# Optimization experiments

Hardware: AMD Instinct MI355X
Metric: run time of the kernel (lower is better)

## Reference

```python
import jax, jax.numpy as jnp
import numpy as np

H = 8          # num_heads
D = 64         # out_dims = input_dims / num_heads
DM = H * D     # input_dims = 512
B, S = 2, 2048


def _linear(x, W, b):
    # torch nn.Linear: x @ W.T + b, W: [out, in]
    return jnp.einsum('...d,ed->...e', x, W) + b


def setup_inputs() -> dict:
    key = jax.random.key(0)
    ks = jax.random.split(key, 12)
    inp = {
        'query': jax.random.normal(ks[0], (B, S, DM), dtype=jnp.float32),
        'key': jax.random.normal(ks[1], (B, S, DM), dtype=jnp.float32),
        'value': jax.random.normal(ks[2], (B, S, DM), dtype=jnp.float32),
        'Wq': jax.random.normal(ks[3], (D, D), dtype=jnp.float32) * 0.02,
        'bq': jnp.zeros((D,), dtype=jnp.float32),
        'Wk': jax.random.normal(ks[4], (D, D), dtype=jnp.float32) * 0.02,
        'bk': jnp.zeros((D,), dtype=jnp.float32),
        'Wv': jax.random.normal(ks[5], (D, D), dtype=jnp.float32) * 0.02,
        'bv': jnp.zeros((D,), dtype=jnp.float32),
        'Wo': jax.random.normal(ks[6], (DM, DM), dtype=jnp.float32) * 0.02,
        'bo': jnp.zeros((DM,), dtype=jnp.float32),
        'mask': jax.random.randint(ks[7], (B, 1, 1, S), 0, 2, dtype=jnp.int32),
    }
    return inp


def reference(query, key, value, Wq, bq, Wk, bk, Wv, bv, Wo, bo, mask):
    b, qlen = query.shape[0], query.shape[1]
    klen = key.shape[1]
    # split heads: [B, S, H, D]
    q = _linear(query.reshape(b, qlen, H, D), Wq, bq)
    k = _linear(key.reshape(b, klen, H, D), Wk, bk)
    v = _linear(value.reshape(b, klen, H, D), Wv, bv)
    # scores: [B, H, Q, K]
    attn = jnp.einsum('bqhd,bkhd->bhqk', q, k)
    attn = jnp.where(mask == 0, jnp.float32(-1e20), attn)
    # NOTE: original scale is num_heads ** 1 / 2 == H / 2 (Python precedence quirk)
    score = jax.nn.softmax(attn * (2.0 / H), axis=-1)
    # out einsum gives [B, Q, D, H]; flattening gives (d, h) feature order
    out = jnp.einsum('bhqv,bvhd->bqdh', score, v)
    out = out.reshape(b, qlen, D * H)
    return _linear(out, Wo, bo)
```

## Files before the change

### kernel.cpp

```cpp
#include <hip/hip_runtime.h>
#include <math.h>

typedef float f32x4 __attribute__((ext_vector_type(4)));
typedef short s16x8 __attribute__((ext_vector_type(8)));
typedef unsigned short ushort_t;

namespace {
constexpr int kH  = 8;
constexpr int kD  = 64;
constexpr int kDM = 512;
constexpr int kB  = 2;
constexpr int kS  = 2048;
constexpr size_t kNE = (size_t)kB * kS * kDM;
constexpr size_t kNL = (size_t)kB * kH * kS;
}

__device__ __forceinline__ void split_bf16(float x, ushort_t& hi, ushort_t& lo) {
  union { float f; unsigned u; } a; a.f = x;
  hi = (ushort_t)(a.u >> 16);
  union { unsigned u; float f; } hh; hh.u = a.u & 0xffff0000u;
  union { float f; unsigned u; } r; r.f = x - hh.f;
  lo = (ushort_t)(r.u >> 16);
}
__device__ __forceinline__ ushort_t rne_bf16(float x) {
  union { float f; unsigned u; } a; a.f = x;
  const unsigned t = a.u + 0x7fffu + ((a.u >> 16) & 1u);
  return (ushort_t)(t >> 16);
}
__device__ __forceinline__ float bf_to_f(unsigned u16) {
  union { unsigned u; float f; } a; a.u = u16 << 16; return a.f;
}

__global__ __launch_bounds__(256)
void w_split_kernel(const float* __restrict__ Wo, const float* __restrict__ Wq,
                    const float* __restrict__ Wk, const float* __restrict__ Wv,
                    ushort_t* __restrict__ wo_h, ushort_t* __restrict__ wo_l,
                    ushort_t* __restrict__ wq_h, ushort_t* __restrict__ wq_l,
                    ushort_t* __restrict__ wk_h, ushort_t* __restrict__ wk_l,
                    ushort_t* __restrict__ wv_h, ushort_t* __restrict__ wv_l) {
  const int bid = blockIdx.x;
  if (bid < 128) {
    const int gi = (bid * 256 + threadIdx.x) * 8;
    const int e  = gi >> 9;
    const int g0 = gi & 511;
    const int fbase = (g0 & 63) * 8 + (g0 >> 6);
    ushort_t h[8], l[8];
    #pragma unroll
    for (int j = 0; j < 8; ++j)
      split_bf16(Wo[(size_t)e * kDM + fbase + j * 8], h[j], l[j]);
    int4 hp, lp;
    hp.x = (int)((unsigned)h[0] | ((unsigned)h[1] << 16));
    hp.y = (int)((unsigned)h[2] | ((unsigned)h[3] << 16));
    hp.z = (int)((unsigned)h[4] | ((unsigned)h[5] << 16));
    hp.w = (int)((unsigned)h[6] | ((unsigned)h[7] << 16));
    lp.x = (int)((unsigned)l[0] | ((unsigned)l[1] << 16));
    lp.y = (int)((unsigned)l[2] | ((unsigned)l[3] << 16));
    lp.z = (int)((unsigned)l[4] | ((unsigned)l[5] << 16));
    lp.w = (int)((unsigned)l[6] | ((unsigned)l[7] << 16));
    *(int4*)&wo_h[(size_t)e * kDM + g0] = hp;
    *(int4*)&wo_l[(size_t)e * kDM + g0] = lp;
  } else {
    const int which = bid - 128;
    const float* W = (which == 0) ? Wq : (which == 1) ? Wk : Wv;
    ushort_t* oh = (which == 0) ? wq_h : (which == 1) ? wk_h : wv_h;
    ushort_t* ol = (which == 0) ? wq_l : (which == 1) ? wk_l : wv_l;
    #pragma unroll
    for (int cc = 0; cc < 4; ++cc) {
      const int i = (cc * 256 + threadIdx.x) * 4;
      const float4 v = *(const float4*)&W[i];
      ushort_t h[4], l[4];
      split_bf16(v.x, h[0], l[0]);
      split_bf16(v.y, h[1], l[1]);
      split_bf16(v.z, h[2], l[2]);
      split_bf16(v.w, h[3], l[3]);
      int2 hp, lp;
      hp.x = (int)((unsigned)h[0] | ((unsigned)h[1] << 16));
      hp.y = (int)((unsigned)h[2] | ((unsigned)h[3] << 16));
      lp.x = (int)((unsigned)l[0] | ((unsigned)l[1] << 16));
      lp.y = (int)((unsigned)l[2] | ((unsigned)l[3] << 16));
      *(int2*)&oh[i] = hp;
      *(int2*)&ol[i] = lp;
    }
  }
}

__global__ __launch_bounds__(256, 2)
void kv_proj_kernel(const float* __restrict__ xk, const float* __restrict__ xv,
                    const ushort_t* __restrict__ wk_h, const ushort_t* __restrict__ wk_l,
                    const float* __restrict__ bk,
                    const ushort_t* __restrict__ wv_h, const ushort_t* __restrict__ wv_l,
                    const float* __restrict__ bv,
                    ushort_t* __restrict__ k_hi, ushort_t* __restrict__ vt_hi) {
  __shared__ __align__(16) ushort_t Xh[64][72];
  __shared__ __align__(16) ushort_t Xl[64][72];
  const int which = blockIdx.z;
  const float* x = which ? xv : xk;
  const ushort_t* wh = which ? wv_h : wk_h;
  const ushort_t* wl = which ? wv_l : wk_l;
  const float* bias = which ? bv : bk;
  const int h = blockIdx.y;
  const int t0g = blockIdx.x * 64;
  const int b = t0g >> 11, s0 = t0g & (kS - 1);
  const int tid  = threadIdx.x;
  const int w    = tid >> 6;
  const int lane = tid & 63;
  const int ln   = lane & 15;
  const int quad = lane >> 4;
  const size_t hb = ((size_t)b * kH + h) * (size_t)(kS * kD);

  #pragma unroll
  for (int cc = 0; cc < 4; ++cc) {
    const int id = tid + cc * 256;
    const int r = id >> 4, c = id & 15;
    const float4 v = *(const float4*)&x[((size_t)t0g + r) * kDM + h * kD + c * 4];
    ushort_t hh[4], ll[4];
    split_bf16(v.x, hh[0], ll[0]);
    split_bf16(v.y, hh[1], ll[1]);
    split_bf16(v.z, hh[2], ll[2]);
    split_bf16(v.w, hh[3], ll[3]);
    int2 hp, lp;
    hp.x = (int)((unsigned)hh[0] | ((unsigned)hh[1] << 16));
    hp.y = (int)((unsigned)hh[2] | ((unsigned)hh[3] << 16));
    lp.x = (int)((unsigned)ll[0] | ((unsigned)ll[1] << 16));
    lp.y = (int)((unsigned)ll[2] | ((unsigned)ll[3] << 16));
    *(int2*)&Xh[r][c * 4] = hp;
    *(int2*)&Xl[r][c * 4] = lp;
  }
  __syncthreads();

  f32x4 C[4];
  #pragma unroll
  for (int eb = 0; eb < 4; ++eb) C[eb] = (f32x4){0.f, 0.f, 0.f, 0.f};
  #pragma unroll
  for (int kc = 0; kc < 2; ++kc) {
    const s16x8 ah = *(const s16x8*)&Xh[w * 16 + ln][kc * 32 + quad * 8];
    const s16x8 al = *(const s16x8*)&Xl[w * 16 + ln][kc * 32 + quad * 8];
    s16x8 bh[4], bl[4];
    #pragma unroll
    for (int eb = 0; eb < 4; ++eb) {
      bh[eb] = *(const s16x8*)&wh[(size_t)(eb * 16 + ln) * kD + kc * 32 + quad * 8];
      bl[eb] = *(const s16x8*)&wl[(size_t)(eb * 16 + ln) * kD + kc * 32 + quad * 8];
    }
    #pragma unroll
    for (int eb = 0; eb < 4; ++eb)
      C[eb] = __builtin_amdgcn_mfma_f32_16x16x32_bf16(ah, bh[eb], C[eb], 0, 0, 0);
    #pragma unroll
    for (int eb = 0; eb < 4; ++eb)
      C[eb] = __builtin_amdgcn_mfma_f32_16x16x32_bf16(ah, bl[eb], C[eb], 0, 0, 0);
    #pragma unroll
    for (int eb = 0; eb < 4; ++eb)
      C[eb] = __builtin_amdgcn_mfma_f32_16x16x32_bf16(al, bh[eb], C[eb], 0, 0, 0);
  }
  __syncthreads();

  if (which == 0) {
    #pragma unroll
    for (int eb = 0; eb < 4; ++eb) {
      const float be = bias[eb * 16 + ln];
      #pragma unroll
      for (int r = 0; r < 4; ++r)
        Xh[w * 16 + quad * 4 + r][eb * 16 + ln] = rne_bf16(C[eb][r] + be);
    }
    __syncthreads();
    #pragma unroll
    for (int cc = 0; cc < 2; ++cc) {
      const int id = tid + cc * 256;
      const int r = id >> 3, c = id & 7;
      *(int4*)&k_hi[hb + (size_t)(s0 + r) * kD + c * 8] = *(int4*)&Xh[r][c * 8];
    }
  } else {
    #pragma unroll
    for (int eb = 0; eb < 4; ++eb) {
      const float be = bias[eb * 16 + ln];
      #pragma unroll
      for (int r = 0; r < 4; ++r)
        Xh[eb * 16 + ln][w * 16 + quad * 4 + r] = rne_bf16(C[eb][r] + be);
    }
    __syncthreads();
    #pragma unroll
    for (int cc = 0; cc < 2; ++cc) {
      const int id = tid + cc * 256;
      const int r = id >> 3, c = id & 7;
      *(int4*)&vt_hi[hb + (size_t)r * kS + s0 + c * 8] = *(int4*)&Xh[r][c * 8];
    }
  }
}

__global__ __launch_bounds__(256, 4)
void attn_kernel(const float* __restrict__ xq,
                 const ushort_t* __restrict__ wq_h, const ushort_t* __restrict__ wq_l,
                 const float* __restrict__ bq,
                 const ushort_t* __restrict__ k_hi, const ushort_t* __restrict__ vt_hi,
                 const int* __restrict__ mask,
                 ushort_t* __restrict__ Opart, float* __restrict__ lws) {
  __shared__ __align__(16) ushort_t smem[128 * 72];
  __shared__ __align__(16) ushort_t Pbm[4 * 32 * 40];
  __shared__ float Mz[64];
  ushort_t (*QT)[72] = (ushort_t(*)[72])smem;
  ushort_t (*Kh)[72] = (ushort_t(*)[72])smem;
  ushort_t (*Vh)[72] = (ushort_t(*)[72])(smem + 64 * 72);
  ushort_t (*Pb)[32][40] = (ushort_t(*)[32][40])Pbm;

  const int tid  = threadIdx.x;
  const int w    = tid >> 6;
  const int lane = tid & 63;
  const int ln   = lane & 15;
  const int quad = lane >> 4;
  const int h    = blockIdx.y;
  const int b    = blockIdx.z >> 2;
  const int quarter = blockIdx.z & 3;
  const int q0   = blockIdx.x * 128;
  const size_t hb = ((size_t)b * kH + h) * (size_t)(kS * kD);

  s16x8 aqh[2][2];
  #pragma unroll
  for (int g = 0; g < 2; ++g) {
    const int qrow = q0 + w * 32 + g * 16 + ln;
    f32x4 C[4];
    #pragma unroll
    for (int eb = 0; eb < 4; ++eb) C[eb] = (f32x4){0.f, 0.f, 0.f, 0.f};
    #pragma unroll
    for (int kc = 0; kc < 2; ++kc) {
      const float* xp = &xq[((size_t)b * kS + qrow) * kDM + h * kD + kc * 32 + quad * 8];
      const float4 x0 = *(const float4*)xp;
      const float4 x1 = *(const float4*)(xp + 4);
      const float xs[8] = {x0.x, x0.y, x0.z, x0.w, x1.x, x1.y, x1.z, x1.w};
      s16x8 ah, al;
      #pragma unroll
      for (int j = 0; j < 8; ++j) {
        ushort_t hi, lo;
        split_bf16(xs[j], hi, lo);
        ah[j] = (short)hi; al[j] = (short)lo;
      }
      #pragma unroll
      for (int eb = 0; eb < 4; ++eb) {
        const s16x8 bh = *(const s16x8*)&wq_h[(size_t)(eb * 16 + ln) * kD + kc * 32 + quad * 8];
        const s16x8 bl = *(const s16x8*)&wq_l[(size_t)(eb * 16 + ln) * kD + kc * 32 + quad * 8];
        C[eb] = __builtin_amdgcn_mfma_f32_16x16x32_bf16(ah, bh, C[eb], 0, 0, 0);
        C[eb] = __builtin_amdgcn_mfma_f32_16x16x32_bf16(ah, bl, C[eb], 0, 0, 0);
        C[eb] = __builtin_amdgcn_mfma_f32_16x16x32_bf16(al, bh, C[eb], 0, 0, 0);
      }
    }
    #pragma unroll
    for (int eb = 0; eb < 4; ++eb) {
      const float be = bq[eb * 16 + ln];
      #pragma unroll
      for (int r = 0; r < 4; ++r)
        QT[w * 32 + g * 16 + quad * 4 + r][eb * 16 + ln] = rne_bf16(C[eb][r] + be);
    }
    #pragma unroll
    for (int db = 0; db < 2; ++db)
      aqh[g][db] = *(const s16x8*)&QT[w * 32 + g * 16 + ln][db * 32 + quad * 8];
  }
  __syncthreads();

  f32x4 O[2][4];
  #pragma unroll
  for (int g = 0; g < 2; ++g)
    #pragma unroll
    for (int db = 0; db < 4; ++db) O[g][db] = (f32x4){0.f, 0.f, 0.f, 0.f};
  float rs[2][4] = {};

  const int kt0 = quarter * 8;
  for (int kt = kt0; kt < kt0 + 8; ++kt) {
    __syncthreads();
    {
      const ushort_t* gkh = k_hi + hb + (size_t)kt * 64 * kD;
      const ushort_t* gvh = vt_hi + hb + (size_t)kt * 64;
      #pragma unroll
      for (int cc = 0; cc < 2; ++cc) {
        const int id = tid + cc * 256;
        const int r = id >> 3, c = id & 7;
        *(int4*)&Kh[r][c * 8] = *(const int4*)&gkh[r * kD + c * 8];
        *(int4*)&Vh[r][c * 8] = *(const int4*)&gvh[(size_t)r * kS + c * 8];
      }
      if (tid < 64) Mz[tid] = (mask[(size_t)b * kS + kt * 64 + tid] != 0) ? 1.0f : 0.0f;
    }
    __syncthreads();

    #pragma unroll
    for (int h32 = 0; h32 < 2; ++h32) {
      f32x4 C[2][2];
      #pragma unroll
      for (int g = 0; g < 2; ++g) {
        C[g][0] = (f32x4){0.f, 0.f, 0.f, 0.f};
        C[g][1] = (f32x4){0.f, 0.f, 0.f, 0.f};
      }
      #pragma unroll
      for (int db = 0; db < 2; ++db) {
        const s16x8 bh0 = *(const s16x8*)&Kh[h32 * 32 + ln][db * 32 + quad * 8];
        const s16x8 bh1 = *(const s16x8*)&Kh[h32 * 32 + 16 + ln][db * 32 + quad * 8];
        #pragma unroll
        for (int g = 0; g < 2; ++g) {
          C[g][0] = __builtin_amdgcn_mfma_f32_16x16x32_bf16(aqh[g][db], bh0, C[g][0], 0, 0, 0);
          C[g][1] = __builtin_amdgcn_mfma_f32_16x16x32_bf16(aqh[g][db], bh1, C[g][1], 0, 0, 0);
        }
      }
      #pragma unroll
      for (int g = 0; g < 2; ++g) {
        #pragma unroll
        for (int kb = 0; kb < 2; ++kb) {
          const float mz = Mz[h32 * 32 + kb * 16 + ln];
          #pragma unroll
          for (int r = 0; r < 4; ++r) {
            const float p = mz * __expf(0.25f * C[g][kb][r]);
            union { float f; unsigned u; } pa; pa.f = p;
            const unsigned t = pa.u + 0x7fffu + ((pa.u >> 16) & 1u);
            Pb[w][g * 16 + quad * 4 + r][kb * 16 + ln] = (ushort_t)(t >> 16);
            union { unsigned u; float f; } pr; pr.u = t & 0xffff0000u;
            rs[g][r] += pr.f;
          }
        }
      }
      {
        const s16x8 ph0 = *(const s16x8*)&Pb[w][ln][quad * 8];
        const s16x8 ph1 = *(const s16x8*)&Pb[w][16 + ln][quad * 8];
        #pragma unroll
        for (int db = 0; db < 4; ++db) {
          const s16x8 vh = *(const s16x8*)&Vh[db * 16 + ln][h32 * 32 + quad * 8];
          O[0][db] = __builtin_amdgcn_mfma_f32_16x16x32_bf16(ph0, vh, O[0][db], 0, 0, 0);
          O[1][db] = __builtin_amdgcn_mfma_f32_16x16x32_bf16(ph1, vh, O[1][db], 0, 0, 0);
        }
      }
    }
  }

  #pragma unroll
  for (int m = 1; m < 16; m <<= 1) {
    #pragma unroll
    for (int g = 0; g < 2; ++g)
      #pragma unroll
      for (int r = 0; r < 4; ++r) rs[g][r] += __shfl_xor(rs[g][r], m);
  }
  if (ln == 0) {
    #pragma unroll
    for (int g = 0; g < 2; ++g) {
      float* lp = lws + (size_t)quarter * kNL + ((size_t)b * kH + h) * kS +
                  q0 + w * 32 + g * 16 + quad * 4;
      #pragma unroll
      for (int r = 0; r < 4; ++r) lp[r] = rs[g][r];
    }
  }

  __syncthreads();
  #pragma unroll
  for (int g = 0; g < 2; ++g)
    #pragma unroll
    for (int db = 0; db < 4; ++db)
      #pragma unroll
      for (int r = 0; r < 4; ++r)
        QT[w * 32 + g * 16 + quad * 4 + r][db * 16 + ln] = rne_bf16(O[g][db][r]);
  __syncthreads();
  ushort_t* op = Opart + (size_t)quarter * kNE;
  #pragma unroll
  for (int cc = 0; cc < 4; ++cc) {
    const int id = tid + cc * 256;
    const int r = id >> 3, c = id & 7;
    *(int4*)&op[((size_t)b * kS + q0 + r) * kDM + h * kD + c * 8] = *(int4*)&QT[r][c * 8];
  }
}

__global__ __launch_bounds__(256, 2)
void out_proj_kernel(const ushort_t* __restrict__ Opart, const float* __restrict__ lws,
                     const ushort_t* __restrict__ wh, const ushort_t* __restrict__ wl,
                     const float* __restrict__ bo, float* __restrict__ out) {
  __shared__ __align__(16) ushort_t Ah[64][72];
  __shared__ __align__(16) ushort_t Al[64][72];
  __shared__ __align__(16) ushort_t Bh[64][72];
  __shared__ __align__(16) ushort_t Bl[64][72];
  __shared__ float linv[kH][64];
  const int t0 = blockIdx.x * 64;
  const int e0 = blockIdx.y * 64;
  const int b  = t0 >> 11;
  const int s0 = t0 & (kS - 1);
  const int tid  = threadIdx.x;
  const int w    = tid >> 6;
  const int lane = tid & 63;
  const int ln   = lane & 15;
  const int quad = lane >> 4;

  for (int id = tid; id < kH * 64; id += 256) {
    const int hh = id >> 6, r = id & 63;
    const size_t base = ((size_t)b * kH + hh) * kS + s0 + r;
    linv[hh][r] = 1.0f / (lws[base] + lws[kNL + base] +
                          lws[2 * kNL + base] + lws[3 * kNL + base]);
  }

  f32x4 C[4];
  #pragma unroll
  for (int eb = 0; eb < 4; ++eb) C[eb] = (f32x4){0.f, 0.f, 0.f, 0.f};

  for (int k0 = 0; k0 < kDM; k0 += 64) {
    __syncthreads();
    const int hh = k0 >> 6;
    #pragma unroll
    for (int cc = 0; cc < 4; ++cc) {
      const int id = tid + cc * 256;
      const int r = id >> 4, c4 = id & 15;
      const size_t off = (size_t)(t0 + r) * kDM + k0 + c4 * 4;
      float a0 = 0.f, a1 = 0.f, a2 = 0.f, a3 = 0.f;
      #pragma unroll
      for (int q = 0; q < 4; ++q) {
        const int2 u = *(const int2*)&Opart[(size_t)q * kNE + off];
        a0 += bf_to_f((unsigned)u.x & 0xffffu);
        a1 += bf_to_f((unsigned)u.x >> 16);
        a2 += bf_to_f((unsigned)u.y & 0xffffu);
        a3 += bf_to_f((unsigned)u.y >> 16);
      }
      const float li = linv[hh][r];
      a0 *= li; a1 *= li; a2 *= li; a3 *= li;
      ushort_t h4[4], l4[4];
      split_bf16(a0, h4[0], l4[0]);
      split_bf16(a1, h4[1], l4[1]);
      split_bf16(a2, h4[2], l4[2]);
      split_bf16(a3, h4[3], l4[3]);
      int2 hp, lp;
      hp.x = (int)((unsigned)h4[0] | ((unsigned)h4[1] << 16));
      hp.y = (int)((unsigned)h4[2] | ((unsigned)h4[3] << 16));
      lp.x = (int)((unsigned)l4[0] | ((unsigned)l4[1] << 16));
      lp.y = (int)((unsigned)l4[2] | ((unsigned)l4[3] << 16));
      *(int2*)&Ah[r][c4 * 4] = hp;
      *(int2*)&Al[r][c4 * 4] = lp;
    }
    #pragma unroll
    for (int cc = 0; cc < 2; ++cc) {
      const int id = tid + cc * 256;
      const int r = id >> 3, off = (id & 7) * 8;
      *(int4*)&Bh[r][off] = *(const int4*)&wh[(size_t)(e0 + r) * kDM + k0 + off];
      *(int4*)&Bl[r][off] = *(const int4*)&wl[(size_t)(e0 + r) * kDM + k0 + off];
    }
    __syncthreads();
    #pragma unroll
    for (int kc = 0; kc < 2; ++kc) {
      const s16x8 ah = *(const s16x8*)&Ah[w * 16 + ln][kc * 32 + quad * 8];
      const s16x8 al = *(const s16x8*)&Al[w * 16 + ln][kc * 32 + quad * 8];
      s16x8 bh[4], bl[4];
      #pragma unroll
      for (int eb = 0; eb < 4; ++eb) {
        bh[eb] = *(const s16x8*)&Bh[eb * 16 + ln][kc * 32 + quad * 8];
        bl[eb] = *(const s16x8*)&Bl[eb * 16 + ln][kc * 32 + quad * 8];
      }
      #pragma unroll
      for (int eb = 0; eb < 4; ++eb)
        C[eb] = __builtin_amdgcn_mfma_f32_16x16x32_bf16(ah, bh[eb], C[eb], 0, 0, 0);
      #pragma unroll
      for (int eb = 0; eb < 4; ++eb)
        C[eb] = __builtin_amdgcn_mfma_f32_16x16x32_bf16(ah, bl[eb], C[eb], 0, 0, 0);
      #pragma unroll
      for (int eb = 0; eb < 4; ++eb)
        C[eb] = __builtin_amdgcn_mfma_f32_16x16x32_bf16(al, bh[eb], C[eb], 0, 0, 0);
    }
  }

  #pragma unroll
  for (int eb = 0; eb < 4; ++eb) {
    const int e = e0 + eb * 16 + ln;
    const float be = bo[e];
    #pragma unroll
    for (int r = 0; r < 4; ++r) {
      const int t = t0 + w * 16 + quad * 4 + r;
      out[(size_t)t * kDM + e] = C[eb][r] + be;
    }
  }
}

extern "C" void kernel_launch(void* const* d_in, const int* in_sizes, int n_in,
                              void* d_out, int out_size, void* d_ws, size_t ws_size,
                              hipStream_t stream) {
  const float* query = (const float*)d_in[0];
  const float* key   = (const float*)d_in[1];
  const float* value = (const float*)d_in[2];
  const float* Wq = (const float*)d_in[3];
  const float* bq = (const float*)d_in[4];
  const float* Wk = (const float*)d_in[5];
  const float* bk = (const float*)d_in[6];
  const float* Wv = (const float*)d_in[7];
  const float* bv = (const float*)d_in[8];
  const float* Wo = (const float*)d_in[9];
  const float* bo = (const float*)d_in[10];
  const int* mask = (const int*)d_in[11];
  float* out = (float*)d_out;

  ushort_t* k_hi  = (ushort_t*)d_ws;
  ushort_t* vt_hi = k_hi + kNE;
  ushort_t* wo_h  = vt_hi + kNE;
  ushort_t* wo_l  = wo_h + (size_t)kDM * kDM;
  ushort_t* Opart = wo_l + (size_t)kDM * kDM;
  float*    lws   = (float*)(Opart + 4 * kNE);
  ushort_t* wq_h  = (ushort_t*)(lws + 4 * kNL);
  ushort_t* wq_l  = wq_h + kD * kD;
  ushort_t* wk_h  = wq_l + kD * kD;
  ushort_t* wk_l  = wk_h + kD * kD;
  ushort_t* wv_h  = wk_l + kD * kD;
  ushort_t* wv_l  = wv_h + kD * kD;

  w_split_kernel<<<dim3(131), 256, 0, stream>>>(
      Wo, Wq, Wk, Wv, wo_h, wo_l, wq_h, wq_l, wk_h, wk_l, wv_h, wv_l);
  kv_proj_kernel<<<dim3(kB * kS / 64, kH, 2), 256, 0, stream>>>(
      key, value, wk_h, wk_l, bk, wv_h, wv_l, bv, k_hi, vt_hi);
  attn_kernel<<<dim3(kS / 128, kH, kB * 4), 256, 0, stream>>>(
      query, wq_h, wq_l, bq, k_hi, vt_hi, mask, Opart, lws);
  out_proj_kernel<<<dim3(kB * kS / 64, kDM / 64), 256, 0, stream>>>(
      Opart, lws, wo_h, wo_l, bo, out);
}
```

Before: 173.6 us.

## Fold weight split into KV projection, drop LDS staging in attention, retile out-proj

Removes the separate weight-split launch by handling the Wo/Wq splitting in an extra z-slice of the KV projection kernel, which now splits Wk/Wv to bf16 hi/lo on the fly from fp32. The attention kernel stops staging K, V and the mask through shared memory with block barriers and reads MFMA fragments straight from global memory. The output projection is retiled to 32x128 tiles with a 32-wide k-step. Together these aim to cut launch overhead and synchronization, at the cost of uncoalesced, redundant global loads in attention and more k-loop iterations in the out-projection.

After: 242.2 us. 1.4x slower.

```diff
diff --git a/kernel.cpp b/kernel.cpp
--- a/kernel.cpp
+++ b/kernel.cpp
@@ -31,72 +31,63 @@
   union { unsigned u; float f; } a; a.u = u16 << 16; return a.f;
 }
 
-__global__ __launch_bounds__(256)
-void w_split_kernel(const float* __restrict__ Wo, const float* __restrict__ Wq,
-                    const float* __restrict__ Wk, const float* __restrict__ Wv,
+__global__ __launch_bounds__(256, 2)
+void kv_proj_kernel(const float* __restrict__ xk, const float* __restrict__ xv,
+                    const float* __restrict__ Wk, const float* __restrict__ bk,
+                    const float* __restrict__ Wv, const float* __restrict__ bv,
+                    const float* __restrict__ Wo, const float* __restrict__ Wq,
                     ushort_t* __restrict__ wo_h, ushort_t* __restrict__ wo_l,
                     ushort_t* __restrict__ wq_h, ushort_t* __restrict__ wq_l,
-                    ushort_t* __restrict__ wk_h, ushort_t* __restrict__ wk_l,
-                    ushort_t* __restrict__ wv_h, ushort_t* __restrict__ wv_l) {
-  const int bid = blockIdx.x;
-  if (bid < 128) {
-    const int gi = (bid * 256 + threadIdx.x) * 8;
-    const int e  = gi >> 9;
-    const int g0 = gi & 511;
-    const int fbase = (g0 & 63) * 8 + (g0 >> 6);
-    ushort_t h[8], l[8];
-    #pragma unroll
-    for (int j = 0; j < 8; ++j)
-      split_bf16(Wo[(size_t)e * kDM + fbase + j * 8], h[j], l[j]);
-    int4 hp, lp;
-    hp.x = (int)((unsigned)h[0] | ((unsigned)h[1] << 16));
-    hp.y = (int)((unsigned)h[2] | ((unsigned)h[3] << 16));
-    hp.z = (int)((unsigned)h[4] | ((unsigned)h[5] << 16));
-    hp.w = (int)((unsigned)h[6] | ((unsigned)h[7] << 16));
-    lp.x = (int)((unsigned)l[0] | ((unsigned)l[1] << 16));
-    lp.y = (int)((unsigned)l[2] | ((unsigned)l[3] << 16));
-    lp.z = (int)((unsigned)l[4] | ((unsigned)l[5] << 16));
-    lp.w = (int)((unsigned)l[6] | ((unsigned)l[7] << 16));
-    *(int4*)&wo_h[(size_t)e * kDM + g0] = hp;
-    *(int4*)&wo_l[(size_t)e * kDM + g0] = lp;
-  } else {
-    const int which = bid - 128;
-    const float* W = (which == 0) ? Wq : (which == 1) ? Wk : Wv;
-    ushort_t* oh = (which == 0) ? wq_h : (which == 1) ? wk_h : wv_h;
-    ushort_t* ol = (which == 0) ? wq_l : (which == 1) ? wk_l : wv_l;
-    #pragma unroll
-    for (int cc = 0; cc < 4; ++cc) {
-      const int i = (cc * 256 + threadIdx.x) * 4;
-      const float4 v = *(const float4*)&W[i];
-      ushort_t h[4], l[4];
-      split_bf16(v.x, h[0], l[0]);
-      split_bf16(v.y, h[1], l[1]);
-      split_bf16(v.z, h[2], l[2]);
-      split_bf16(v.w, h[3], l[3]);
-      int2 hp, lp;
-      hp.x = (int)((unsigned)h[0] | ((unsigned)h[1] << 16));
-      hp.y = (int)((unsigned)h[2] | ((unsigned)h[3] << 16));
-      lp.x = (int)((unsigned)l[0] | ((unsigned)l[1] << 16));
-      lp.y = (int)((unsigned)l[2] | ((unsigned)l[3] << 16));
-      *(int2*)&oh[i] = hp;
-      *(int2*)&ol[i] = lp;
-    }
-  }
-}
-
-__global__ __launch_bounds__(256, 2)
-void kv_proj_kernel(const float* __restrict__ xk, const float* __restrict__ xv,
-                    const ushort_t* __restrict__ wk_h, const ushort_t* __restrict__ wk_l,
-                    const float* __restrict__ bk,
-                    const ushort_t* __restrict__ wv_h, const ushort_t* __restrict__ wv_l,
-                    const float* __restrict__ bv,
                     ushort_t* __restrict__ k_hi, ushort_t* __restrict__ vt_hi) {
+  const int which = blockIdx.z;
+  if (which == 2) {
+    const int bid = blockIdx.y * 64 + blockIdx.x;
+    if (bid < 128) {
+      const int gi = (bid * 256 + threadIdx.x) * 8;
+      const int e  = gi >> 9;
+      const int g0 = gi & 511;
+      const int fbase = (g0 & 63) * 8 + (g0 >> 6);
+      ushort_t h8[8], l8[8];
+      #pragma unroll
+      for (int j = 0; j < 8; ++j)
+        split_bf16(Wo[(size_t)e * kDM + fbase + j * 8], h8[j], l8[j]);
+      int4 hp, lp;
+      hp.x = (int)((unsigned)h8[0] | ((unsigned)h8[1] << 16));
+      hp.y = (int)((unsigned)h8[2] | ((unsigned)h8[3] << 16));
+      hp.z = (int)((unsigned)h8[4] | ((unsigned)h8[5] << 16));
+      hp.w = (int)((unsigned)h8[6] | ((unsigned)h8[7] << 16));
+      lp.x = (int)((unsigned)l8[0] | ((unsigned)l8[1] << 16));
+      lp.y = (int)((unsigned)l8[2] | ((unsigned)l8[3] << 16));
+      lp.z = (int)((unsigned)l8[4] | ((unsigned)l8[5] << 16));
+      lp.w = (int)((unsigned)l8[6] | ((unsigned)l8[7] << 16));
+      *(int4*)&wo_h[(size_t)e * kDM + g0] = hp;
+      *(int4*)&wo_l[(size_t)e * kDM + g0] = lp;
+    } else if (bid == 128) {
+      #pragma unroll
+      for (int cc = 0; cc < 4; ++cc) {
+        const int i = (cc * 256 + threadIdx.x) * 4;
+        const float4 v = *(const float4*)&Wq[i];
+        ushort_t h4[4], l4[4];
+        split_bf16(v.x, h4[0], l4[0]);
+        split_bf16(v.y, h4[1], l4[1]);
+        split_bf16(v.z, h4[2], l4[2]);
+        split_bf16(v.w, h4[3], l4[3]);
+        int2 hp, lp;
+        hp.x = (int)((unsigned)h4[0] | ((unsigned)h4[1] << 16));
+        hp.y = (int)((unsigned)h4[2] | ((unsigned)h4[3] << 16));
+        lp.x = (int)((unsigned)l4[0] | ((unsigned)l4[1] << 16));
+        lp.y = (int)((unsigned)l4[2] | ((unsigned)l4[3] << 16));
+        *(int2*)&wq_h[i] = hp;
+        *(int2*)&wq_l[i] = lp;
+      }
+    }
+    return;
+  }
+
   __shared__ __align__(16) ushort_t Xh[64][72];
   __shared__ __align__(16) ushort_t Xl[64][72];
-  const int which = blockIdx.z;
   const float* x = which ? xv : xk;
-  const ushort_t* wh = which ? wv_h : wk_h;
-  const ushort_t* wl = which ? wv_l : wk_l;
+  const float* W = which ? Wv : Wk;
   const float* bias = which ? bv : bk;
   const int h = blockIdx.y;
   const int t0g = blockIdx.x * 64;
@@ -135,21 +126,23 @@
   for (int kc = 0; kc < 2; ++kc) {
     const s16x8 ah = *(const s16x8*)&Xh[w * 16 + ln][kc * 32 + quad * 8];
     const s16x8 al = *(const s16x8*)&Xl[w * 16 + ln][kc * 32 + quad * 8];
-    s16x8 bh[4], bl[4];
     #pragma unroll
     for (int eb = 0; eb < 4; ++eb) {
-      bh[eb] = *(const s16x8*)&wh[(size_t)(eb * 16 + ln) * kD + kc * 32 + quad * 8];
-      bl[eb] = *(const s16x8*)&wl[(size_t)(eb * 16 + ln) * kD + kc * 32 + quad * 8];
-    }
-    #pragma unroll
-    for (int eb = 0; eb < 4; ++eb)
-      C[eb] = __builtin_amdgcn_mfma_f32_16x16x32_bf16(ah, bh[eb], C[eb], 0, 0, 0);
-    #pragma unroll
-    for (int eb = 0; eb < 4; ++eb)
-      C[eb] = __builtin_amdgcn_mfma_f32_16x16x32_bf16(ah, bl[eb], C[eb], 0, 0, 0);
-    #pragma unroll
-    for (int eb = 0; eb < 4; ++eb)
-      C[eb] = __builtin_amdgcn_mfma_f32_16x16x32_bf16(al, bh[eb], C[eb], 0, 0, 0);
+      const float* wp = &W[(size_t)(eb * 16 + ln) * kD + kc * 32 + quad * 8];
+      const float4 w0 = *(const float4*)wp;
+      const float4 w1 = *(const float4*)(wp + 4);
+      const float ws[8] = {w0.x, w0.y, w0.z, w0.w, w1.x, w1.y, w1.z, w1.w};
+      s16x8 bh, bl;
+      #pragma unroll
+      for (int j = 0; j < 8; ++j) {
+        ushort_t hi, lo;
+        split_bf16(ws[j], hi, lo);
+        bh[j] = (short)hi; bl[j] = (short)lo;
+      }
+      C[eb] = __builtin_amdgcn_mfma_f32_16x16x32_bf16(ah, bh, C[eb], 0, 0, 0);
+      C[eb] = __builtin_amdgcn_mfma_f32_16x16x32_bf16(ah, bl, C[eb], 0, 0, 0);
+      C[eb] = __builtin_amdgcn_mfma_f32_16x16x32_bf16(al, bh, C[eb], 0, 0, 0);
+    }
   }
   __syncthreads();
 
@@ -193,13 +186,8 @@
                  const ushort_t* __restrict__ k_hi, const ushort_t* __restrict__ vt_hi,
                  const int* __restrict__ mask,
                  ushort_t* __restrict__ Opart, float* __restrict__ lws) {
-  __shared__ __align__(16) ushort_t smem[128 * 72];
-  __shared__ __align__(16) ushort_t Pbm[4 * 32 * 40];
-  __shared__ float Mz[64];
-  ushort_t (*QT)[72] = (ushort_t(*)[72])smem;
-  ushort_t (*Kh)[72] = (ushort_t(*)[72])smem;
-  ushort_t (*Vh)[72] = (ushort_t(*)[72])(smem + 64 * 72);
-  ushort_t (*Pb)[32][40] = (ushort_t(*)[32][40])Pbm;
+  __shared__ __align__(16) ushort_t QT[128][72];
+  __shared__ __align__(16) ushort_t Pb[4][32][40];
 
   const int tid  = threadIdx.x;
   const int w    = tid >> 6;
@@ -252,7 +240,6 @@
     for (int db = 0; db < 2; ++db)
       aqh[g][db] = *(const s16x8*)&QT[w * 32 + g * 16 + ln][db * 32 + quad * 8];
   }
-  __syncthreads();
 
   f32x4 O[2][4];
   #pragma unroll
@@ -263,23 +250,19 @@
 
   const int kt0 = quarter * 8;
   for (int kt = kt0; kt < kt0 + 8; ++kt) {
-    __syncthreads();
-    {
-      const ushort_t* gkh = k_hi + hb + (size_t)kt * 64 * kD;
-      const ushort_t* gvh = vt_hi + hb + (size_t)kt * 64;
-      #pragma unroll
-      for (int cc = 0; cc < 2; ++cc) {
-        const int id = tid + cc * 256;
-        const int r = id >> 3, c = id & 7;
-        *(int4*)&Kh[r][c * 8] = *(const int4*)&gkh[r * kD + c * 8];
-        *(int4*)&Vh[r][c * 8] = *(const int4*)&gvh[(size_t)r * kS + c * 8];
-      }
-      if (tid < 64) Mz[tid] = (mask[(size_t)b * kS + kt * 64 + tid] != 0) ? 1.0f : 0.0f;
-    }
-    __syncthreads();
-
     #pragma unroll
     for (int h32 = 0; h32 < 2; ++h32) {
+      const int keybase = kt * 64 + h32 * 32;
+      s16x8 kf[2][2];
+      #pragma unroll
+      for (int kb = 0; kb < 2; ++kb)
+        #pragma unroll
+        for (int db = 0; db < 2; ++db)
+          kf[kb][db] = *(const s16x8*)
+              &k_hi[hb + (size_t)(keybase + kb * 16 + ln) * kD + db * 32 + quad * 8];
+      const float mz0 = (mask[(size_t)b * kS + keybase + ln] != 0) ? 1.0f : 0.0f;
+      const float mz1 = (mask[(size_t)b * kS + keybase + 16 + ln] != 0) ? 1.0f : 0.0f;
+
       f32x4 C[2][2];
       #pragma unroll
       for (int g = 0; g < 2; ++g) {
@@ -287,20 +270,17 @@
         C[g][1] = (f32x4){0.f, 0.f, 0.f, 0.f};
       }
       #pragma unroll
-      for (int db = 0; db < 2; ++db) {
-        const s16x8 bh0 = *(const s16x8*)&Kh[h32 * 32 + ln][db * 32 + quad * 8];
-        const s16x8 bh1 = *(const s16x8*)&Kh[h32 * 32 + 16 + ln][db * 32 + quad * 8];
+      for (int db = 0; db < 2; ++db)
         #pragma unroll
         for (int g = 0; g < 2; ++g) {
-          C[g][0] = __builtin_amdgcn_mfma_f32_16x16x32_bf16(aqh[g][db], bh0, C[g][0], 0, 0, 0);
-          C[g][1] = __builtin_amdgcn_mfma_f32_16x16x32_bf16(aqh[g][db], bh1, C[g][1], 0, 0, 0);
+          C[g][0] = __builtin_amdgcn_mfma_f32_16x16x32_bf16(aqh[g][db], kf[0][db], C[g][0], 0, 0, 0);
+          C[g][1] = __builtin_amdgcn_mfma_f32_16x16x32_bf16(aqh[g][db], kf[1][db], C[g][1], 0, 0, 0);
         }
-      }
       #pragma unroll
       for (int g = 0; g < 2; ++g) {
         #pragma unroll
         for (int kb = 0; kb < 2; ++kb) {
-          const float mz = Mz[h32 * 32 + kb * 16 + ln];
+          const float mz = kb ? mz1 : mz0;
           #pragma unroll
           for (int r = 0; r < 4; ++r) {
             const float p = mz * __expf(0.25f * C[g][kb][r]);
@@ -312,15 +292,17 @@
           }
         }
       }
-      {
-        const s16x8 ph0 = *(const s16x8*)&Pb[w][ln][quad * 8];
-        const s16x8 ph1 = *(const s16x8*)&Pb[w][16 + ln][quad * 8];
-        #pragma unroll
-        for (int db = 0; db < 4; ++db) {
-          const s16x8 vh = *(const s16x8*)&Vh[db * 16 + ln][h32 * 32 + quad * 8];
-          O[0][db] = __builtin_amdgcn_mfma_f32_16x16x32_bf16(ph0, vh, O[0][db], 0, 0, 0);
-          O[1][db] = __builtin_amdgcn_mfma_f32_16x16x32_bf16(ph1, vh, O[1][db], 0, 0, 0);
-        }
+      s16x8 vf[4];
+      #pragma unroll
+      for (int db = 0; db < 4; ++db)
+        vf[db] = *(const s16x8*)
+            &vt_hi[hb + (size_t)(db * 16 + ln) * kS + keybase + quad * 8];
+      const s16x8 ph0 = *(const s16x8*)&Pb[w][ln][quad * 8];
+      const s16x8 ph1 = *(const s16x8*)&Pb[w][16 + ln][quad * 8];
+      #pragma unroll
+      for (int db = 0; db < 4; ++db) {
+        O[0][db] = __builtin_amdgcn_mfma_f32_16x16x32_bf16(ph0, vf[db], O[0][db], 0, 0, 0);
+        O[1][db] = __builtin_amdgcn_mfma_f32_16x16x32_bf16(ph1, vf[db], O[1][db], 0, 0, 0);
       }
     }
   }
@@ -342,7 +324,6 @@
     }
   }
 
-  __syncthreads();
   #pragma unroll
   for (int g = 0; g < 2; ++g)
     #pragma unroll
@@ -364,13 +345,13 @@
 void out_proj_kernel(const ushort_t* __restrict__ Opart, const float* __restrict__ lws,
                      const ushort_t* __restrict__ wh, const ushort_t* __restrict__ wl,
                      const float* __restrict__ bo, float* __restrict__ out) {
-  __shared__ __align__(16) ushort_t Ah[64][72];
-  __shared__ __align__(16) ushort_t Al[64][72];
-  __shared__ __align__(16) ushort_t Bh[64][72];
-  __shared__ __align__(16) ushort_t Bl[64][72];
-  __shared__ float linv[kH][64];
-  const int t0 = blockIdx.x * 64;
-  const int e0 = blockIdx.y * 64;
+  __shared__ __align__(16) ushort_t Ah[32][40];
+  __shared__ __align__(16) ushort_t Al[32][40];
+  __shared__ __align__(16) ushort_t Bh[128][40];
+  __shared__ __align__(16) ushort_t Bl[128][40];
+  __shared__ float linv[kH][32];
+  const int t0 = blockIdx.x * 32;
+  const int e0 = blockIdx.y * 128;
   const int b  = t0 >> 11;
   const int s0 = t0 & (kS - 1);
   const int tid  = threadIdx.x;
@@ -378,9 +359,11 @@
   const int lane = tid & 63;
   const int ln   = lane & 15;
   const int quad = lane >> 4;
-
-  for (int id = tid; id < kH * 64; id += 256) {
-    const int hh = id >> 6, r = id & 63;
+  const int tsub = w & 1;
+  const int esub = w >> 1;
+
+  {
+    const int hh = tid >> 5, r = tid & 31;
     const size_t base = ((size_t)b * kH + hh) * kS + s0 + r;
     linv[hh][r] = 1.0f / (lws[base] + lws[kNL + base] +
                           lws[2 * kNL + base] + lws[3 * kNL + base]);
@@ -390,14 +373,12 @@
   #pragma unroll
   for (int eb = 0; eb < 4; ++eb) C[eb] = (f32x4){0.f, 0.f, 0.f, 0.f};
 
-  for (int k0 = 0; k0 < kDM; k0 += 64) {
+  for (int k0 = 0; k0 < kDM; k0 += 32) {
     __syncthreads();
     const int hh = k0 >> 6;
-    #pragma unroll
-    for (int cc = 0; cc < 4; ++cc) {
-      const int id = tid + cc * 256;
-      const int r = id >> 4, c4 = id & 15;
-      const size_t off = (size_t)(t0 + r) * kDM + k0 + c4 * 4;
+    {
+      const int r = tid >> 3, c4 = (tid & 7) * 4;
+      const size_t off = (size_t)(t0 + r) * kDM + k0 + c4;
       float a0 = 0.f, a1 = 0.f, a2 = 0.f, a3 = 0.f;
       #pragma unroll
       for (int q = 0; q < 4; ++q) {
@@ -419,46 +400,36 @@
       hp.y = (int)((unsigned)h4[2] | ((unsigned)h4[3] << 16));
       lp.x = (int)((unsigned)l4[0] | ((unsigned)l4[1] << 16));
       lp.y = (int)((unsigned)l4[2] | ((unsigned)l4[3] << 16));
-      *(int2*)&Ah[r][c4 * 4] = hp;
-      *(int2*)&Al[r][c4 * 4] = lp;
+      *(int2*)&Ah[r][c4] = hp;
+      *(int2*)&Al[r][c4] = lp;
     }
     #pragma unroll
     for (int cc = 0; cc < 2; ++cc) {
       const int id = tid + cc * 256;
-      const int r = id >> 3, off = (id & 7) * 8;
-      *(int4*)&Bh[r][off] = *(const int4*)&wh[(size_t)(e0 + r) * kDM + k0 + off];
-      *(int4*)&Bl[r][off] = *(const int4*)&wl[(size_t)(e0 + r) * kDM + k0 + off];
+      const int r = id >> 2, c = (id & 3) * 8;
+      *(int4*)&Bh[r][c] = *(const int4*)&wh[(size_t)(e0 + r) * kDM + k0 + c];
+      *(int4*)&Bl[r][c] = *(const int4*)&wl[(size_t)(e0 + r) * kDM + k0 + c];
     }
     __syncthreads();
-    #pragma unroll
-    for (int kc = 0; kc < 2; ++kc) {
-      const s16x8 ah = *(const s16x8*)&Ah[w * 16 + ln][kc * 32 + quad * 8];
-      const s16x8 al = *(const s16x8*)&Al[w * 16 + ln][kc * 32 + quad * 8];
-      s16x8 bh[4], bl[4];
-      #pragma unroll
-      for (int eb = 0; eb < 4; ++eb) {
-        bh[eb] = *(const s16x8*)&Bh[eb * 16 + ln][kc * 32 + quad * 8];
-        bl[eb] = *(const s16x8*)&Bl[eb * 16 + ln][kc * 32 + quad * 8];
-      }
-      #pragma unroll
-      for (int eb = 0; eb < 4; ++eb)
-        C[eb] = __builtin_amdgcn_mfma_f32_16x16x32_bf16(ah, bh[eb], C[eb], 0, 0, 0);
-      #pragma unroll
-      for (int eb = 0; eb < 4; ++eb)
-        C[eb] = __builtin_amdgcn_mfma_f32_16x16x32_bf16(ah, bl[eb], C[eb], 0, 0, 0);
-      #pragma unroll
-      for (int eb = 0; eb < 4; ++eb)
-        C[eb] = __builtin_amdgcn_mfma_f32_16x16x32_bf16(al, bh[eb], C[eb], 0, 0, 0);
+    const s16x8 ah = *(const s16x8*)&Ah[tsub * 16 + ln][quad * 8];
+    const s16x8 al = *(const s16x8*)&Al[tsub * 16 + ln][quad * 8];
+    #pragma unroll
+    for (int eb = 0; eb < 4; ++eb) {
+      const s16x8 bh = *(const s16x8*)&Bh[esub * 64 + eb * 16 + ln][quad * 8];
+      const s16x8 bl = *(const s16x8*)&Bl[esub * 64 + eb * 16 + ln][quad * 8];
+      C[eb] = __builtin_amdgcn_mfma_f32_16x16x32_bf16(ah, bh, C[eb], 0, 0, 0);
+      C[eb] = __builtin_amdgcn_mfma_f32_16x16x32_bf16(ah, bl, C[eb], 0, 0, 0);
+      C[eb] = __builtin_amdgcn_mfma_f32_16x16x32_bf16(al, bh, C[eb], 0, 0, 0);
     }
   }
 
   #pragma unroll
   for (int eb = 0; eb < 4; ++eb) {
-    const int e = e0 + eb * 16 + ln;
+    const int e = e0 + esub * 64 + eb * 16 + ln;
     const float be = bo[e];
     #pragma unroll
     for (int r = 0; r < 4; ++r) {
-      const int t = t0 + w * 16 + quad * 4 + r;
+      const int t = t0 + tsub * 16 + quad * 4 + r;
       out[(size_t)t * kDM + e] = C[eb][r] + be;
     }
   }
@@ -489,17 +460,11 @@
   float*    lws   = (float*)(Opart + 4 * kNE);
   ushort_t* wq_h  = (ushort_t*)(lws + 4 * kNL);
   ushort_t* wq_l  = wq_h + kD * kD;
-  ushort_t* wk_h  = wq_l + kD * kD;
-  ushort_t* wk_l  = wk_h + kD * kD;
-  ushort_t* wv_h  = wk_l + kD * kD;
-  ushort_t* wv_l  = wv_h + kD * kD;
-
-  w_split_kernel<<<dim3(131), 256, 0, stream>>>(
-      Wo, Wq, Wk, Wv, wo_h, wo_l, wq_h, wq_l, wk_h, wk_l, wv_h, wv_l);
-  kv_proj_kernel<<<dim3(kB * kS / 64, kH, 2), 256, 0, stream>>>(
-      key, value, wk_h, wk_l, bk, wv_h, wv_l, bv, k_hi, vt_hi);
+
+  kv_proj_kernel<<<dim3(kB * kS / 64, kH, 3), 256, 0, stream>>>(
+      key, value, Wk, bk, Wv, bv, Wo, Wq, wo_h, wo_l, wq_h, wq_l, k_hi, vt_hi);
   attn_kernel<<<dim3(kS / 128, kH, kB * 4), 256, 0, stream>>>(
       query, wq_h, wq_l, bq, k_hi, vt_hi, mask, Opart, lws);
-  out_proj_kernel<<<dim3(kB * kS / 64, kDM / 64), 256, 0, stream>>>(
+  out_proj_kernel<<<dim3(kB * kS / 32, kDM / 128), 256, 0, stream>>>(
       Opart, lws, wo_h, wo_l, bo, out);
 }
```
